# Kernel optimization log

Measured on AMD Instinct MI355X. Metric: run time of the kernel, lower is better.

Reference implementation:

```python
import jax, jax.numpy as jnp
import numpy as np
import math

N = 100000
E = 3200000
D_IN = 512
HID = 512
N_CLASSES = 64


def _uniform_param(key, shape, fan_out):
    std = 1.0 / math.sqrt(fan_out)
    return jax.random.uniform(key, shape, dtype=jnp.float32, minval=-std, maxval=std)


def setup_inputs() -> dict:
    key = jax.random.key(0)
    ks = jax.random.split(key, 12)
    X = jax.random.normal(ks[0], (N, D_IN), dtype=jnp.float32)
    edge_src = jax.random.randint(ks[1], (E,), 0, N, dtype=jnp.int32)
    edge_dst = jax.random.randint(ks[2], (E,), 0, N, dtype=jnp.int32)
    edge_w = jax.random.uniform(ks[3], (E,), dtype=jnp.float32)
    # layer sizes: [D_IN] + hidden_layers + [N_CLASSES]
    W0 = _uniform_param(ks[4], (D_IN, HID), HID)
    b0 = _uniform_param(ks[5], (HID,), HID)
    W1 = _uniform_param(ks[6], (HID, HID), HID)
    b1 = _uniform_param(ks[7], (HID,), HID)
    W2 = _uniform_param(ks[8], (HID, N_CLASSES), N_CLASSES)
    b2 = _uniform_param(ks[9], (N_CLASSES,), N_CLASSES)
    return {
        "X": X, "edge_src": edge_src, "edge_dst": edge_dst, "edge_w": edge_w,
        "W0": W0, "b0": b0, "W1": W1, "b1": b1, "W2": W2, "b2": b2,
    }


def _spmm(edge_src, edge_dst, edge_w, H):
    # out[i] = sum_{edges (i<-j)} w * H[j]; rows = edge_dst, cols = edge_src
    msgs = edge_w[:, None] * H[edge_src]          # [E, K]
    return jax.ops.segment_sum(msgs, edge_dst, num_segments=N)


def _gcn_layer(edge_src, edge_dst, edge_w, H, W, b):
    H = H @ W                                      # [N, out]
    H = _spmm(edge_src, edge_dst, edge_w, H)
    return H + b


def reference(X, edge_src, edge_dst, edge_w, W0, b0, W1, b1, W2, b2):
    # inference mode: dropout is identity (training=False)
    H = _gcn_layer(edge_src, edge_dst, edge_w, X, W0, b0)
    H = jax.nn.relu(H)
    H = _gcn_layer(edge_src, edge_dst, edge_w, H, W1, b1)
    H = jax.nn.relu(H)
    H = _gcn_layer(edge_src, edge_dst, edge_w, H, W2, b2)
    return jax.nn.softmax(H, axis=-1)              # [N, C]
```

## Files before the change

### kernel.cpp

```cpp
#include <hip/hip_runtime.h>
#include <hip/hip_bf16.h>
#include <cstdint>
#include <cstddef>

#define GN 100000
#define GE 3200000

typedef __attribute__((ext_vector_type(8))) _Float16 f16x8;
typedef __attribute__((ext_vector_type(4))) _Float16 f16x4;
typedef __attribute__((ext_vector_type(4))) float f32x4;


__global__ void k_zero(int* __restrict__ p, int n) {
    int i = blockIdx.x * blockDim.x + threadIdx.x;
    if (i < n) p[i] = 0;
}

__global__ void k_hist(const int* __restrict__ dst, int* __restrict__ cnt, int e) {
    for (int i = blockIdx.x * blockDim.x + threadIdx.x; i < e; i += gridDim.x * blockDim.x)
        atomicAdd(&cnt[dst[i]], 1);
}

__global__ void k_chunksum(const int* __restrict__ cnt, int* __restrict__ bsum, int n) {
    __shared__ int s[256];
    int b = blockIdx.x, t = threadIdx.x;
    int i0 = b * 512;
    int v = 0;
    int i1 = i0 + t;        if (i1 < n) v += cnt[i1];
    int i2 = i0 + 256 + t;  if (i2 < n) v += cnt[i2];
    s[t] = v; __syncthreads();
    for (int d = 128; d > 0; d >>= 1) {
        if (t < d) s[t] += s[t + d];
        __syncthreads();
    }
    if (t == 0) bsum[b] = s[0];
}

__global__ void k_scanb(const int* __restrict__ bsum, int* __restrict__ boff, int nb,
                        int* __restrict__ row_ptr, int n) {
    if (threadIdx.x == 0 && blockIdx.x == 0) {
        int acc = 0;
        for (int b = 0; b < nb; b++) { boff[b] = acc; acc += bsum[b]; }
        row_ptr[n] = acc;
    }
}

__global__ void k_scanw(const int* __restrict__ cnt, const int* __restrict__ boff,
                        int* __restrict__ row_ptr, int* __restrict__ cursor, int n) {
    __shared__ int s[512];
    int b = blockIdx.x, t = threadIdx.x;
    int i = b * 512 + t;
    int x = (i < n) ? cnt[i] : 0;
    s[t] = x; __syncthreads();
    for (int d = 1; d < 512; d <<= 1) {
        int v = (t >= d) ? s[t - d] : 0;
        __syncthreads();
        s[t] += v;
        __syncthreads();
    }
    int excl = s[t] - x + boff[b];
    if (i < n) { row_ptr[i] = excl; cursor[i] = excl; }
}

__global__ void k_scatter(const int* __restrict__ src, const int* __restrict__ dst,
                          const float* __restrict__ w, int* __restrict__ cursor,
                          int* __restrict__ ecol, float* __restrict__ ew, int e) {
    for (int i = blockIdx.x * blockDim.x + threadIdx.x; i < e; i += gridDim.x * blockDim.x) {
        int d = dst[i];
        int p = atomicAdd(&cursor[d], 1);
        ecol[p] = src[i];
        ew[p]   = w[i];
    }
}


__global__ void k_transp_split(const float* __restrict__ W,
                               _Float16* __restrict__ Wth, _Float16* __restrict__ Wtl,
                               int K, int M) {
    __shared__ float tile[32][33];
    int bx = blockIdx.x * 32;
    int by = blockIdx.y * 32;
    int tx = threadIdx.x, ty = threadIdx.y;
    for (int i = ty; i < 32; i += 8)
        tile[i][tx] = W[(size_t)(by + i) * M + bx + tx];
    __syncthreads();
    for (int i = ty; i < 32; i += 8) {
        float w = tile[tx][i];
        _Float16 h = (_Float16)w;
        _Float16 l = (_Float16)(w - (float)h);
        Wth[(size_t)(bx + i) * K + by + tx] = h;
        Wtl[(size_t)(bx + i) * K + by + tx] = l;
    }
}


template<int BN, typename OutT>
__global__ __launch_bounds__(256, 2) void k_gemm_split(const float* __restrict__ A,
                                                       const _Float16* __restrict__ Bth,
                                                       const _Float16* __restrict__ Btl,
                                                       OutT* __restrict__ C,
                                                       int n, int m) {
    constexpr int NI  = BN / 32;
    constexpr int BIT = BN / 32;
    __shared__ _Float16 Ash[128 * 64];
    __shared__ _Float16 Asl[128 * 64];
    __shared__ _Float16 Bsh[BN * 64];
    __shared__ _Float16 Bsl[BN * 64];
    int tid = threadIdx.x;
    int wv = tid >> 6, lane = tid & 63;
    int wr = wv >> 1, wc = wv & 1;
    int r0 = blockIdx.y * 128;
    int c0 = blockIdx.x * BN;

    float4 areg[8];
    f16x8 bregh[BIT], bregl[BIT];
    f32x4 acc[4][NI];
    #pragma unroll
    for (int i = 0; i < 4; i++)
        #pragma unroll
        for (int j = 0; j < NI; j++)
            acc[i][j] = (f32x4){0.f, 0.f, 0.f, 0.f};

    auto aload = [&](int kt) {
        #pragma unroll
        for (int i = 0; i < 8; ++i) {
            int q = tid + 256 * i;
            int row = q >> 4, c4 = q & 15;
            int gr = r0 + row; if (gr >= n) gr = n - 1;
            areg[i] = *(const float4*)(A + (size_t)gr * 512 + kt * 64 + c4 * 4);
        }
        #pragma unroll
        for (int i = 0; i < BIT; ++i) {
            int q = tid + 256 * i;
            int col = q >> 3, c = q & 7;
            size_t off = (size_t)(c0 + col) * 512 + kt * 64 + c * 8;
            bregh[i] = *(const f16x8*)(Bth + off);
            bregl[i] = *(const f16x8*)(Btl + off);
        }
    };

    aload(0);
    for (int kt = 0; kt < 8; ++kt) {
        __syncthreads();
        #pragma unroll
        for (int i = 0; i < 8; ++i) {
            int q = tid + 256 * i;
            int row = q >> 4, c4 = q & 15;
            int g = c4 ^ ((row & 7) << 1);
            float4 a = areg[i];
            _Float16 hx = (_Float16)a.x, hy = (_Float16)a.y;
            _Float16 hz = (_Float16)a.z, hw = (_Float16)a.w;
            f16x4 h = { hx, hy, hz, hw };
            f16x4 l = { (_Float16)(a.x - (float)hx), (_Float16)(a.y - (float)hy),
                        (_Float16)(a.z - (float)hz), (_Float16)(a.w - (float)hw) };
            *(f16x4*)&Ash[row * 64 + g * 4] = h;
            *(f16x4*)&Asl[row * 64 + g * 4] = l;
        }
        #pragma unroll
        for (int i = 0; i < BIT; ++i) {
            int q = tid + 256 * i;
            int col = q >> 3, c = q & 7;
            int idx = col * 64 + ((c ^ (col & 7)) * 8);
            *(f16x8*)&Bsh[idx] = bregh[i];
            *(f16x8*)&Bsl[idx] = bregl[i];
        }
        __syncthreads();
        if (kt < 7) aload(kt + 1);
        #pragma unroll
        for (int ks = 0; ks < 2; ++ks) {
            f16x8 afh[4], afl[4], bfh[NI], bfl[NI];
            int cch = ks * 4 + (lane >> 4);
            #pragma unroll
            for (int mi = 0; mi < 4; ++mi) {
                int row = wr * 64 + mi * 16 + (lane & 15);
                int idx = row * 64 + (((cch * 2) ^ ((row & 7) << 1)) * 4);
                afh[mi] = *(const f16x8*)&Ash[idx];
                afl[mi] = *(const f16x8*)&Asl[idx];
            }
            #pragma unroll
            for (int ni = 0; ni < NI; ++ni) {
                int col = wc * (BN / 2) + ni * 16 + (lane & 15);
                int idx = col * 64 + ((cch ^ (col & 7)) * 8);
                bfh[ni] = *(const f16x8*)&Bsh[idx];
                bfl[ni] = *(const f16x8*)&Bsl[idx];
            }
            #pragma unroll
            for (int mi = 0; mi < 4; ++mi)
                #pragma unroll
                for (int ni = 0; ni < NI; ++ni) {
                    acc[mi][ni] = __builtin_amdgcn_mfma_f32_16x16x32_f16(
                        afh[mi], bfl[ni], acc[mi][ni], 0, 0, 0);
                    acc[mi][ni] = __builtin_amdgcn_mfma_f32_16x16x32_f16(
                        afl[mi], bfh[ni], acc[mi][ni], 0, 0, 0);
                    acc[mi][ni] = __builtin_amdgcn_mfma_f32_16x16x32_f16(
                        afh[mi], bfh[ni], acc[mi][ni], 0, 0, 0);
                }
        }
    }

    #pragma unroll
    for (int mi = 0; mi < 4; ++mi) {
        #pragma unroll
        for (int j = 0; j < 4; ++j) {
            int gr = r0 + wr * 64 + mi * 16 + (lane >> 4) * 4 + j;
            if (gr < n) {
                #pragma unroll
                for (int ni = 0; ni < NI; ++ni) {
                    int gc = c0 + wc * (BN / 2) + ni * 16 + (lane & 15);
                    C[(size_t)gr * m + gc] = (OutT)acc[mi][ni][j];
                }
            }
        }
    }
}


__global__ __launch_bounds__(64) void k_spmm512_h2f(const int* __restrict__ rowp,
                                                    const int* __restrict__ ecol,
                                                    const float* __restrict__ ew,
                                                    const _Float16* __restrict__ H,
                                                    const float* __restrict__ bias,
                                                    float* __restrict__ out,
                                                    int relu) {
    int row = blockIdx.x;
    int t = threadIdx.x;
    int s0 = rowp[row], s1 = rowp[row + 1];
    const f16x8* H8 = (const f16x8*)H;
    float a0 = 0.f, a1 = 0.f, a2 = 0.f, a3 = 0.f;
    float a4 = 0.f, a5 = 0.f, a6 = 0.f, a7 = 0.f;
    __shared__ int   lc[64];
    __shared__ float lw[64];
    for (int base = s0; base < s1; base += 64) {
        int nn = s1 - base; if (nn > 64) nn = 64;
        __syncthreads();
        if (t < nn) {
            lc[t] = __builtin_nontemporal_load(ecol + base + t);
            lw[t] = __builtin_nontemporal_load(ew + base + t);
        }
        __syncthreads();
        int e = 0;
        for (; e + 4 <= nn; e += 4) {
            f16x8 h0 = H8[(size_t)lc[e]     * 64 + t]; float w0 = lw[e];
            f16x8 h1 = H8[(size_t)lc[e + 1] * 64 + t]; float w1 = lw[e + 1];
            f16x8 h2 = H8[(size_t)lc[e + 2] * 64 + t]; float w2 = lw[e + 2];
            f16x8 h3 = H8[(size_t)lc[e + 3] * 64 + t]; float w3 = lw[e + 3];
            a0 += w0 * (float)h0[0] + w1 * (float)h1[0] + w2 * (float)h2[0] + w3 * (float)h3[0];
            a1 += w0 * (float)h0[1] + w1 * (float)h1[1] + w2 * (float)h2[1] + w3 * (float)h3[1];
            a2 += w0 * (float)h0[2] + w1 * (float)h1[2] + w2 * (float)h2[2] + w3 * (float)h3[2];
            a3 += w0 * (float)h0[3] + w1 * (float)h1[3] + w2 * (float)h2[3] + w3 * (float)h3[3];
            a4 += w0 * (float)h0[4] + w1 * (float)h1[4] + w2 * (float)h2[4] + w3 * (float)h3[4];
            a5 += w0 * (float)h0[5] + w1 * (float)h1[5] + w2 * (float)h2[5] + w3 * (float)h3[5];
            a6 += w0 * (float)h0[6] + w1 * (float)h1[6] + w2 * (float)h2[6] + w3 * (float)h3[6];
            a7 += w0 * (float)h0[7] + w1 * (float)h1[7] + w2 * (float)h2[7] + w3 * (float)h3[7];
        }
        for (; e < nn; ++e) {
            f16x8 h = H8[(size_t)lc[e] * 64 + t]; float w = lw[e];
            a0 += w * (float)h[0]; a1 += w * (float)h[1];
            a2 += w * (float)h[2]; a3 += w * (float)h[3];
            a4 += w * (float)h[4]; a5 += w * (float)h[5];
            a6 += w * (float)h[6]; a7 += w * (float)h[7];
        }
    }
    const float4* b4 = (const float4*)bias;
    float4 blo = b4[t * 2], bhi = b4[t * 2 + 1];
    a0 += blo.x; a1 += blo.y; a2 += blo.z; a3 += blo.w;
    a4 += bhi.x; a5 += bhi.y; a6 += bhi.z; a7 += bhi.w;
    if (relu) {
        a0 = fmaxf(a0, 0.f); a1 = fmaxf(a1, 0.f); a2 = fmaxf(a2, 0.f); a3 = fmaxf(a3, 0.f);
        a4 = fmaxf(a4, 0.f); a5 = fmaxf(a5, 0.f); a6 = fmaxf(a6, 0.f); a7 = fmaxf(a7, 0.f);
    }
    f32x4 o1 = { a0, a1, a2, a3 };
    f32x4 o2 = { a4, a5, a6, a7 };
    f32x4* op = (f32x4*)(out + (size_t)row * 512);
    __builtin_nontemporal_store(o1, op + t * 2);
    __builtin_nontemporal_store(o2, op + t * 2 + 1);
}


__global__ __launch_bounds__(256) void k_spmm64_softmax(const int* __restrict__ rowp,
                                                        const int* __restrict__ ecol,
                                                        const float* __restrict__ ew,
                                                        const float* __restrict__ H,
                                                        const float* __restrict__ bias,
                                                        float* __restrict__ out, int n) {
    int wid  = threadIdx.x >> 6;
    int lane = threadIdx.x & 63;
    int row  = blockIdx.x * 4 + wid;
    if (row >= n) return;
    int s0 = rowp[row], s1 = rowp[row + 1];
    float acc = 0.f;
    int e = s0;
    for (; e + 2 <= s1; e += 2) {
        int   c0 = ecol[e], c1 = ecol[e + 1];
        float w0 = ew[e],   w1 = ew[e + 1];
        acc += w0 * H[(size_t)c0 * 64 + lane] + w1 * H[(size_t)c1 * 64 + lane];
    }
    if (e < s1) acc += ew[e] * H[(size_t)ecol[e] * 64 + lane];
    acc += bias[lane];
    float m = acc;
    for (int d = 32; d > 0; d >>= 1) m = fmaxf(m, __shfl_xor(m, d));
    float p = __expf(acc - m);
    float s = p;
    for (int d = 32; d > 0; d >>= 1) s += __shfl_xor(s, d);
    __builtin_nontemporal_store(p / s, out + (size_t)row * 64 + lane);
}


extern "C" void kernel_launch(void* const* d_in, const int* in_sizes, int n_in,
                              void* d_out, int out_size, void* d_ws, size_t ws_size,
                              hipStream_t stream) {
    const float* X    = (const float*)d_in[0];
    const int*   esrc = (const int*)d_in[1];
    const int*   edst = (const int*)d_in[2];
    const float* ewin = (const float*)d_in[3];
    const float* W0   = (const float*)d_in[4];
    const float* b0   = (const float*)d_in[5];
    const float* W1   = (const float*)d_in[6];
    const float* b1   = (const float*)d_in[7];
    const float* W2   = (const float*)d_in[8];
    const float* b2   = (const float*)d_in[9];
    float* out = (float*)d_out;

    const int N = GN;
    const int E = GE;

    uint8_t* p = (uint8_t*)d_ws;
    auto alloc = [&](size_t bytes) -> void* {
        void* r = (void*)p;
        p += (bytes + 255) & ~(size_t)255;
        return r;
    };
    _Float16* bufM  = (_Float16*)alloc((size_t)N * 512 * 2);
    float*    bufG  = (float*)alloc((size_t)N * 512 * 4);
    float*    bufC3 = (float*)alloc((size_t)N * 64 * 4);
    _Float16* W0th  = (_Float16*)alloc((size_t)512 * 512 * 2);
    _Float16* W0tl  = (_Float16*)alloc((size_t)512 * 512 * 2);
    _Float16* W1th  = (_Float16*)alloc((size_t)512 * 512 * 2);
    _Float16* W1tl  = (_Float16*)alloc((size_t)512 * 512 * 2);
    _Float16* W2th  = (_Float16*)alloc((size_t)64 * 512 * 2);
    _Float16* W2tl  = (_Float16*)alloc((size_t)64 * 512 * 2);
    int*   cnt     = (int*)alloc((size_t)N * 4);
    int*   row_ptr = (int*)alloc((size_t)(N + 1) * 4);
    int*   cursor  = (int*)alloc((size_t)N * 4);
    int*   ecol    = (int*)alloc((size_t)E * 4);
    float* ewv     = (float*)alloc((size_t)E * 4);
    int*   bsum    = (int*)alloc(1024 * 4);
    int*   boff    = (int*)alloc(1024 * 4);

    int nch = (N + 511) / 512;
    k_zero<<<(N + 255) / 256, 256, 0, stream>>>(cnt, N);
    k_hist<<<2048, 256, 0, stream>>>(edst, cnt, E);
    k_chunksum<<<nch, 256, 0, stream>>>(cnt, bsum, N);
    k_scanb<<<1, 64, 0, stream>>>(bsum, boff, nch, row_ptr, N);
    k_scanw<<<nch, 512, 0, stream>>>(cnt, boff, row_ptr, cursor, N);
    k_scatter<<<2048, 256, 0, stream>>>(esrc, edst, ewin, cursor, ecol, ewv, E);

    k_transp_split<<<dim3(16, 16), dim3(32, 8), 0, stream>>>(W0, W0th, W0tl, 512, 512);
    k_transp_split<<<dim3(16, 16), dim3(32, 8), 0, stream>>>(W1, W1th, W1tl, 512, 512);
    k_transp_split<<<dim3(2, 16),  dim3(32, 8), 0, stream>>>(W2, W2th, W2tl, 512, 64);

    int gy = (N + 127) / 128;
    k_gemm_split<128, _Float16><<<dim3(4, gy), 256, 0, stream>>>(X, W0th, W0tl, bufM, N, 512);
    k_spmm512_h2f<<<N, 64, 0, stream>>>(row_ptr, ecol, ewv, bufM, b0, bufG, 1);
    k_gemm_split<128, _Float16><<<dim3(4, gy), 256, 0, stream>>>(bufG, W1th, W1tl, bufM, N, 512);
    k_spmm512_h2f<<<N, 64, 0, stream>>>(row_ptr, ecol, ewv, bufM, b1, bufG, 1);
    k_gemm_split<64, float><<<dim3(1, gy), 256, 0, stream>>>(bufG, W2th, W2tl, bufC3, N, 64);
    k_spmm64_softmax<<<(N + 3) / 4, 256, 0, stream>>>(row_ptr, ecol, ewv, bufC3, b2, out, N);
}
```

Before: 1.896 ms.

## Store intermediate activations in fp16 and add fp16-A GEMM with split weights

The SpMM outputs for layers 1 and 2 are now written as fp16 instead of fp32. A new GEMM kernel reads fp16 activations directly and keeps the hi/lo split only on the weights, halving the MFMA count on the A side. The final 64-wide projection is also stored in fp16, and the gather loops are unrolled further (8 edges per step in the 512-wide SpMM, 4 in the 64-wide one). Together these cut the memory traffic of writing and rereading the intermediate activations, at the cost of fp16 rounding error on activations.

```diff
diff --git a/kernel.cpp b/kernel.cpp
--- a/kernel.cpp
+++ b/kernel.cpp
@@ -215,12 +215,119 @@
 }
 
 
-__global__ __launch_bounds__(64) void k_spmm512_h2f(const int* __restrict__ rowp,
+template<int BN, typename OutT>
+__global__ __launch_bounds__(256, 2) void k_gemm_f16w2(const _Float16* __restrict__ A,
+                                                       const _Float16* __restrict__ Bth,
+                                                       const _Float16* __restrict__ Btl,
+                                                       OutT* __restrict__ C,
+                                                       int n, int m) {
+    constexpr int NI  = BN / 32;
+    constexpr int BIT = BN / 32;
+    __shared__ _Float16 As[128 * 64];
+    __shared__ _Float16 Bsh[BN * 64];
+    __shared__ _Float16 Bsl[BN * 64];
+    int tid = threadIdx.x;
+    int wv = tid >> 6, lane = tid & 63;
+    int wr = wv >> 1, wc = wv & 1;
+    int r0 = blockIdx.y * 128;
+    int c0 = blockIdx.x * BN;
+
+    f16x8 areg[4], bregh[BIT], bregl[BIT];
+    f32x4 acc[4][NI];
+    #pragma unroll
+    for (int i = 0; i < 4; i++)
+        #pragma unroll
+        for (int j = 0; j < NI; j++)
+            acc[i][j] = (f32x4){0.f, 0.f, 0.f, 0.f};
+
+    auto aload = [&](int kt) {
+        #pragma unroll
+        for (int i = 0; i < 4; ++i) {
+            int q = tid + 256 * i;
+            int row = q >> 3, c = q & 7;
+            int gr = r0 + row; if (gr >= n) gr = n - 1;
+            areg[i] = *(const f16x8*)(A + (size_t)gr * 512 + kt * 64 + c * 8);
+        }
+        #pragma unroll
+        for (int i = 0; i < BIT; ++i) {
+            int q = tid + 256 * i;
+            int col = q >> 3, c = q & 7;
+            size_t off = (size_t)(c0 + col) * 512 + kt * 64 + c * 8;
+            bregh[i] = *(const f16x8*)(Bth + off);
+            bregl[i] = *(const f16x8*)(Btl + off);
+        }
+    };
+
+    aload(0);
+    for (int kt = 0; kt < 8; ++kt) {
+        __syncthreads();
+        #pragma unroll
+        for (int i = 0; i < 4; ++i) {
+            int q = tid + 256 * i;
+            int row = q >> 3, c = q & 7;
+            *(f16x8*)&As[row * 64 + ((c ^ (row & 7)) * 8)] = areg[i];
+        }
+        #pragma unroll
+        for (int i = 0; i < BIT; ++i) {
+            int q = tid + 256 * i;
+            int col = q >> 3, c = q & 7;
+            int idx = col * 64 + ((c ^ (col & 7)) * 8);
+            *(f16x8*)&Bsh[idx] = bregh[i];
+            *(f16x8*)&Bsl[idx] = bregl[i];
+        }
+        __syncthreads();
+        if (kt < 7) aload(kt + 1);
+        #pragma unroll
+        for (int ks = 0; ks < 2; ++ks) {
+            f16x8 af[4], bfh[NI], bfl[NI];
+            int cch = ks * 4 + (lane >> 4);
+            #pragma unroll
+            for (int mi = 0; mi < 4; ++mi) {
+                int row = wr * 64 + mi * 16 + (lane & 15);
+                af[mi] = *(const f16x8*)&As[row * 64 + ((cch ^ (row & 7)) * 8)];
+            }
+            #pragma unroll
+            for (int ni = 0; ni < NI; ++ni) {
+                int col = wc * (BN / 2) + ni * 16 + (lane & 15);
+                int idx = col * 64 + ((cch ^ (col & 7)) * 8);
+                bfh[ni] = *(const f16x8*)&Bsh[idx];
+                bfl[ni] = *(const f16x8*)&Bsl[idx];
+            }
+            #pragma unroll
+            for (int mi = 0; mi < 4; ++mi)
+                #pragma unroll
+                for (int ni = 0; ni < NI; ++ni) {
+                    acc[mi][ni] = __builtin_amdgcn_mfma_f32_16x16x32_f16(
+                        af[mi], bfl[ni], acc[mi][ni], 0, 0, 0);
+                    acc[mi][ni] = __builtin_amdgcn_mfma_f32_16x16x32_f16(
+                        af[mi], bfh[ni], acc[mi][ni], 0, 0, 0);
+                }
+        }
+    }
+
+    #pragma unroll
+    for (int mi = 0; mi < 4; ++mi) {
+        #pragma unroll
+        for (int j = 0; j < 4; ++j) {
+            int gr = r0 + wr * 64 + mi * 16 + (lane >> 4) * 4 + j;
+            if (gr < n) {
+                #pragma unroll
+                for (int ni = 0; ni < NI; ++ni) {
+                    int gc = c0 + wc * (BN / 2) + ni * 16 + (lane & 15);
+                    C[(size_t)gr * m + gc] = (OutT)acc[mi][ni][j];
+                }
+            }
+        }
+    }
+}
+
+
+__global__ __launch_bounds__(64) void k_spmm512_h2h(const int* __restrict__ rowp,
                                                     const int* __restrict__ ecol,
                                                     const float* __restrict__ ew,
                                                     const _Float16* __restrict__ H,
                                                     const float* __restrict__ bias,
-                                                    float* __restrict__ out,
+                                                    _Float16* __restrict__ out,
                                                     int relu) {
     int row = blockIdx.x;
     int t = threadIdx.x;
@@ -239,19 +346,33 @@
         }
         __syncthreads();
         int e = 0;
-        for (; e + 4 <= nn; e += 4) {
-            f16x8 h0 = H8[(size_t)lc[e]     * 64 + t]; float w0 = lw[e];
-            f16x8 h1 = H8[(size_t)lc[e + 1] * 64 + t]; float w1 = lw[e + 1];
-            f16x8 h2 = H8[(size_t)lc[e + 2] * 64 + t]; float w2 = lw[e + 2];
-            f16x8 h3 = H8[(size_t)lc[e + 3] * 64 + t]; float w3 = lw[e + 3];
-            a0 += w0 * (float)h0[0] + w1 * (float)h1[0] + w2 * (float)h2[0] + w3 * (float)h3[0];
-            a1 += w0 * (float)h0[1] + w1 * (float)h1[1] + w2 * (float)h2[1] + w3 * (float)h3[1];
-            a2 += w0 * (float)h0[2] + w1 * (float)h1[2] + w2 * (float)h2[2] + w3 * (float)h3[2];
-            a3 += w0 * (float)h0[3] + w1 * (float)h1[3] + w2 * (float)h2[3] + w3 * (float)h3[3];
-            a4 += w0 * (float)h0[4] + w1 * (float)h1[4] + w2 * (float)h2[4] + w3 * (float)h3[4];
-            a5 += w0 * (float)h0[5] + w1 * (float)h1[5] + w2 * (float)h2[5] + w3 * (float)h3[5];
-            a6 += w0 * (float)h0[6] + w1 * (float)h1[6] + w2 * (float)h2[6] + w3 * (float)h3[6];
-            a7 += w0 * (float)h0[7] + w1 * (float)h1[7] + w2 * (float)h2[7] + w3 * (float)h3[7];
+        for (; e + 8 <= nn; e += 8) {
+            f16x8 h0 = H8[(size_t)lc[e]     * 64 + t];
+            f16x8 h1 = H8[(size_t)lc[e + 1] * 64 + t];
+            f16x8 h2 = H8[(size_t)lc[e + 2] * 64 + t];
+            f16x8 h3 = H8[(size_t)lc[e + 3] * 64 + t];
+            f16x8 h4 = H8[(size_t)lc[e + 4] * 64 + t];
+            f16x8 h5 = H8[(size_t)lc[e + 5] * 64 + t];
+            f16x8 h6 = H8[(size_t)lc[e + 6] * 64 + t];
+            f16x8 h7 = H8[(size_t)lc[e + 7] * 64 + t];
+            float w0 = lw[e],     w1 = lw[e + 1], w2 = lw[e + 2], w3 = lw[e + 3];
+            float w4 = lw[e + 4], w5 = lw[e + 5], w6 = lw[e + 6], w7 = lw[e + 7];
+            a0 += w0*(float)h0[0] + w1*(float)h1[0] + w2*(float)h2[0] + w3*(float)h3[0]
+                + w4*(float)h4[0] + w5*(float)h5[0] + w6*(float)h6[0] + w7*(float)h7[0];
+            a1 += w0*(float)h0[1] + w1*(float)h1[1] + w2*(float)h2[1] + w3*(float)h3[1]
+                + w4*(float)h4[1] + w5*(float)h5[1] + w6*(float)h6[1] + w7*(float)h7[1];
+            a2 += w0*(float)h0[2] + w1*(float)h1[2] + w2*(float)h2[2] + w3*(float)h3[2]
+                + w4*(float)h4[2] + w5*(float)h5[2] + w6*(float)h6[2] + w7*(float)h7[2];
+            a3 += w0*(float)h0[3] + w1*(float)h1[3] + w2*(float)h2[3] + w3*(float)h3[3]
+                + w4*(float)h4[3] + w5*(float)h5[3] + w6*(float)h6[3] + w7*(float)h7[3];
+            a4 += w0*(float)h0[4] + w1*(float)h1[4] + w2*(float)h2[4] + w3*(float)h3[4]
+                + w4*(float)h4[4] + w5*(float)h5[4] + w6*(float)h6[4] + w7*(float)h7[4];
+            a5 += w0*(float)h0[5] + w1*(float)h1[5] + w2*(float)h2[5] + w3*(float)h3[5]
+                + w4*(float)h4[5] + w5*(float)h5[5] + w6*(float)h6[5] + w7*(float)h7[5];
+            a6 += w0*(float)h0[6] + w1*(float)h1[6] + w2*(float)h2[6] + w3*(float)h3[6]
+                + w4*(float)h4[6] + w5*(float)h5[6] + w6*(float)h6[6] + w7*(float)h7[6];
+            a7 += w0*(float)h0[7] + w1*(float)h1[7] + w2*(float)h2[7] + w3*(float)h3[7]
+                + w4*(float)h4[7] + w5*(float)h5[7] + w6*(float)h6[7] + w7*(float)h7[7];
         }
         for (; e < nn; ++e) {
             f16x8 h = H8[(size_t)lc[e] * 64 + t]; float w = lw[e];
@@ -269,18 +390,16 @@
         a0 = fmaxf(a0, 0.f); a1 = fmaxf(a1, 0.f); a2 = fmaxf(a2, 0.f); a3 = fmaxf(a3, 0.f);
         a4 = fmaxf(a4, 0.f); a5 = fmaxf(a5, 0.f); a6 = fmaxf(a6, 0.f); a7 = fmaxf(a7, 0.f);
     }
-    f32x4 o1 = { a0, a1, a2, a3 };
-    f32x4 o2 = { a4, a5, a6, a7 };
-    f32x4* op = (f32x4*)(out + (size_t)row * 512);
-    __builtin_nontemporal_store(o1, op + t * 2);
-    __builtin_nontemporal_store(o2, op + t * 2 + 1);
+    f16x8 o = { (_Float16)a0, (_Float16)a1, (_Float16)a2, (_Float16)a3,
+                (_Float16)a4, (_Float16)a5, (_Float16)a6, (_Float16)a7 };
+    ((f16x8*)out)[(size_t)row * 64 + t] = o;
 }
 
 
 __global__ __launch_bounds__(256) void k_spmm64_softmax(const int* __restrict__ rowp,
                                                         const int* __restrict__ ecol,
                                                         const float* __restrict__ ew,
-                                                        const float* __restrict__ H,
+                                                        const _Float16* __restrict__ H,
                                                         const float* __restrict__ bias,
                                                         float* __restrict__ out, int n) {
     int wid  = threadIdx.x >> 6;
@@ -290,12 +409,15 @@
     int s0 = rowp[row], s1 = rowp[row + 1];
     float acc = 0.f;
     int e = s0;
-    for (; e + 2 <= s1; e += 2) {
-        int   c0 = ecol[e], c1 = ecol[e + 1];
-        float w0 = ew[e],   w1 = ew[e + 1];
-        acc += w0 * H[(size_t)c0 * 64 + lane] + w1 * H[(size_t)c1 * 64 + lane];
-    }
-    if (e < s1) acc += ew[e] * H[(size_t)ecol[e] * 64 + lane];
+    for (; e + 4 <= s1; e += 4) {
+        float h0 = (float)H[(size_t)ecol[e]     * 64 + lane];
+        float h1 = (float)H[(size_t)ecol[e + 1] * 64 + lane];
+        float h2 = (float)H[(size_t)ecol[e + 2] * 64 + lane];
+        float h3 = (float)H[(size_t)ecol[e + 3] * 64 + lane];
+        acc += ew[e] * h0 + ew[e + 1] * h1 + ew[e + 2] * h2 + ew[e + 3] * h3;
+    }
+    for (; e < s1; ++e)
+        acc += ew[e] * (float)H[(size_t)ecol[e] * 64 + lane];
     acc += bias[lane];
     float m = acc;
     for (int d = 32; d > 0; d >>= 1) m = fmaxf(m, __shfl_xor(m, d));
@@ -331,8 +453,8 @@
         return r;
     };
     _Float16* bufM  = (_Float16*)alloc((size_t)N * 512 * 2);
-    float*    bufG  = (float*)alloc((size_t)N * 512 * 4);
-    float*    bufC3 = (float*)alloc((size_t)N * 64 * 4);
+    _Float16* bufG  = (_Float16*)alloc((size_t)N * 512 * 2);
+    _Float16* bufC3 = (_Float16*)alloc((size_t)N * 64 * 2);
     _Float16* W0th  = (_Float16*)alloc((size_t)512 * 512 * 2);
     _Float16* W0tl  = (_Float16*)alloc((size_t)512 * 512 * 2);
     _Float16* W1th  = (_Float16*)alloc((size_t)512 * 512 * 2);
@@ -361,9 +483,9 @@
 
     int gy = (N + 127) / 128;
     k_gemm_split<128, _Float16><<<dim3(4, gy), 256, 0, stream>>>(X, W0th, W0tl, bufM, N, 512);
-    k_spmm512_h2f<<<N, 64, 0, stream>>>(row_ptr, ecol, ewv, bufM, b0, bufG, 1);
-    k_gemm_split<128, _Float16><<<dim3(4, gy), 256, 0, stream>>>(bufG, W1th, W1tl, bufM, N, 512);
-    k_spmm512_h2f<<<N, 64, 0, stream>>>(row_ptr, ecol, ewv, bufM, b1, bufG, 1);
-    k_gemm_split<64, float><<<dim3(1, gy), 256, 0, stream>>>(bufG, W2th, W2tl, bufC3, N, 64);
+    k_spmm512_h2h<<<N, 64, 0, stream>>>(row_ptr, ecol, ewv, bufM, b0, bufG, 1);
+    k_gemm_f16w2<128, _Float16><<<dim3(4, gy), 256, 0, stream>>>(bufG, W1th, W1tl, bufM, N, 512);
+    k_spmm512_h2h<<<N, 64, 0, stream>>>(row_ptr, ecol, ewv, bufM, b1, bufG, 1);
+    k_gemm_f16w2<64, _Float16><<<dim3(1, gy), 256, 0, stream>>>(bufG, W2th, W2tl, bufC3, N, 64);
     k_spmm64_softmax<<<(N + 3) / 4, 256, 0, stream>>>(row_ptr, ecol, ewv, bufC3, b2, out, N);
 }
```

Measured after the change: 1.709 ms. 9.9% less time.
